# Kernel optimization log

Measured on AMD Instinct MI355X. Metric: run time of the kernel, lower is better.

The kernel has to match this reference:

```python
import jax, jax.numpy as jnp
import numpy as np

N, C, INTER = 8192, 256, 128


def setup_inputs() -> dict:
    key = jax.random.key(0)
    ks = jax.random.split(key, 9)
    s_in = 1.0 / np.sqrt(C)
    s_mid = 1.0 / np.sqrt(INTER)
    return {
        "x": jax.random.normal(ks[0], (N, C), dtype=jnp.float32),
        # weights stored [in, out] so projection is x @ w + b
        "g_w": jax.random.uniform(ks[1], (C, INTER), jnp.float32, -s_in, s_in),
        "g_b": jax.random.uniform(ks[2], (INTER,), jnp.float32, -s_in, s_in),
        "theta_w": jax.random.uniform(ks[3], (C, INTER), jnp.float32, -s_in, s_in),
        "theta_b": jax.random.uniform(ks[4], (INTER,), jnp.float32, -s_in, s_in),
        "phi_w": jax.random.uniform(ks[5], (C, INTER), jnp.float32, -s_in, s_in),
        "phi_b": jax.random.uniform(ks[6], (INTER,), jnp.float32, -s_in, s_in),
        "W_w": jax.random.uniform(ks[7], (INTER, C), jnp.float32, -s_mid, s_mid),
        "W_b": jax.random.uniform(ks[8], (C,), jnp.float32, -s_mid, s_mid),
    }


def reference(x, g_w, g_b, theta_w, theta_b, phi_w, phi_b, W_w, W_b):
    # embedded_gaussian variant; dropout treated as eval-mode identity
    g_x = x @ g_w + g_b            # [N, inter]
    theta_x = x @ theta_w + theta_b  # [N, inter]
    phi_x = x @ phi_w + phi_b        # [N, inter]
    f = theta_x @ phi_x.T            # [N, N] score matrix
    f_div_C = jax.nn.softmax(f, axis=-1)
    y = f_div_C @ g_x                # [N, inter]
    W_y = y @ W_w + W_b              # [N, C]
    return W_y + x
```

## Files before the change

kernel.cpp:

```cpp
#include <hip/hip_runtime.h>


typedef __bf16 bf16x8 __attribute__((ext_vector_type(8)));
typedef __bf16 bf16x4 __attribute__((ext_vector_type(4)));
typedef float f32x16 __attribute__((ext_vector_type(16)));

#define DEV __device__ __forceinline__

constexpr int NROW = 8192;
constexpr int CDIM = 256;
constexpr int DI   = 128;
constexpr int KVS  = 16;
constexpr int NIT  = NROW / KVS / 64;
constexpr float MFIX = 32.0f;
constexpr float LOG2E = 1.44269504f;

DEV int crow(int r, int h) { return (r & 3) + 8 * (r >> 2) + 4 * h; }

DEV f32x16 mfma(bf16x8 a, bf16x8 b, f32x16 c) {
    return __builtin_amdgcn_mfma_f32_32x32x16_bf16(a, b, c, 0, 0, 0);
}

DEV unsigned pack2(float a, float b) {
    union { __bf16 h[2]; unsigned u; } t;
    t.h[0] = (__bf16)a; t.h[1] = (__bf16)b;
    return t.u;
}

DEV void dma16(const void* g, void* l) {
    __builtin_amdgcn_global_load_lds(
        (const __attribute__((address_space(1))) unsigned*)g,
        (__attribute__((address_space(3))) unsigned*)l, 16, 0, 0);
}

__global__ void prep_wT(const float* __restrict__ thw, const float* __restrict__ phw,
                        const float* __restrict__ gw,  const float* __restrict__ Ww,
                        __bf16* __restrict__ thT, __bf16* __restrict__ phT,
                        __bf16* __restrict__ gT,  __bf16* __restrict__ WwT)
{
    const int m = blockIdx.y;
    const int o = blockIdx.x * 256 + threadIdx.x;
    if (m < 3) {
        const float* in = m == 0 ? thw : m == 1 ? phw : gw;
        __bf16* out = m == 0 ? thT : m == 1 ? phT : gT;
        int n = o >> 8, kk = o & 255;
        out[o] = (__bf16)in[kk * DI + n];
    } else {
        int c = o >> 7, kk = o & 127;
        WwT[o] = (__bf16)Ww[kk * CDIM + c];
    }
}

__global__ __launch_bounds__(256) void proj3(
    const float* __restrict__ x,
    const __bf16* __restrict__ thT, const float* __restrict__ thb,
    const __bf16* __restrict__ phT, const float* __restrict__ phb,
    const __bf16* __restrict__ gT,  const float* __restrict__ gb,
    __bf16* __restrict__ qo, __bf16* __restrict__ ko, __bf16* __restrict__ vT)
{
    const int which = blockIdx.y;
    const __bf16* wt  = which == 0 ? thT : which == 1 ? phT : gT;
    const float* bias = which == 0 ? thb : which == 1 ? phb : gb;
    const float osc   = which == 0 ? LOG2E : 1.0f;

    const int tid = threadIdx.x;
    const int wv = tid >> 6, lane = tid & 63, l31 = lane & 31, h = lane >> 5;
    const int rsel = wv & 1, csel = wv >> 1;

    if (which < 2) {
        __bf16* out = which == 0 ? qo : ko;
        const int row0 = blockIdx.x * 64 + rsel * 32;
        f32x16 acc[2] = {};
#pragma unroll
        for (int kk = 0; kk < 16; ++kk) {
            const float4* xp = (const float4*)(x + (size_t)(row0 + l31) * CDIM + kk * 16 + h * 8);
            float4 a0 = xp[0], a1 = xp[1];
            bf16x8 af;
            af[0] = (__bf16)a0.x; af[1] = (__bf16)a0.y; af[2] = (__bf16)a0.z; af[3] = (__bf16)a0.w;
            af[4] = (__bf16)a1.x; af[5] = (__bf16)a1.y; af[6] = (__bf16)a1.z; af[7] = (__bf16)a1.w;
#pragma unroll
            for (int jn = 0; jn < 2; ++jn) {
                int col0 = csel * 64 + jn * 32;
                bf16x8 bfr = *(const bf16x8*)(wt + (size_t)(col0 + l31) * CDIM + kk * 16 + h * 8);
                acc[jn] = mfma(af, bfr, acc[jn]);
            }
        }
#pragma unroll
        for (int jn = 0; jn < 2; ++jn) {
            int col = csel * 64 + jn * 32 + l31;
            float bv = bias[col];
#pragma unroll
            for (int r = 0; r < 16; ++r)
                out[(size_t)(row0 + crow(r, h)) * DI + col] = (__bf16)((acc[jn][r] + bv) * osc);
        }
    } else {
        const int xr0 = blockIdx.x * 64 + rsel * 32;
        f32x16 acc[2] = {};
#pragma unroll
        for (int kk = 0; kk < 16; ++kk) {
            const float4* xp = (const float4*)(x + (size_t)(xr0 + l31) * CDIM + kk * 16 + h * 8);
            float4 b0 = xp[0], b1 = xp[1];
            bf16x8 bf;
            bf[0] = (__bf16)b0.x; bf[1] = (__bf16)b0.y; bf[2] = (__bf16)b0.z; bf[3] = (__bf16)b0.w;
            bf[4] = (__bf16)b1.x; bf[5] = (__bf16)b1.y; bf[6] = (__bf16)b1.z; bf[7] = (__bf16)b1.w;
#pragma unroll
            for (int jn = 0; jn < 2; ++jn) {
                int i0 = csel * 64 + jn * 32;
                bf16x8 afr = *(const bf16x8*)(wt + (size_t)(i0 + l31) * CDIM + kk * 16 + h * 8);
                acc[jn] = mfma(afr, bf, acc[jn]);
            }
        }
#pragma unroll
        for (int jn = 0; jn < 2; ++jn) {
            int i0 = csel * 64 + jn * 32;
#pragma unroll
            for (int r = 0; r < 16; ++r) {
                int i = i0 + crow(r, h);
                vT[(size_t)i * NROW + xr0 + l31] = (__bf16)(acc[jn][r] + bias[i]);
            }
        }
    }
}

__global__ __launch_bounds__(256, 2) void flash(
    const __bf16* __restrict__ q, const __bf16* __restrict__ k,
    const __bf16* __restrict__ vT, __bf16* __restrict__ yac,
    float* __restrict__ mll)
{
    __shared__ __align__(16) __bf16 KtA[2][64 * 128];
    __shared__ __align__(16) __bf16 VtA[2][64 * 128];

    const int tid = threadIdx.x;
    const int wv = tid >> 6, lane = tid & 63, l31 = lane & 31, h = lane >> 5;
    const int bid = blockIdx.x;
    const int sp = bid & 15, qt = bid >> 4;
    const int q0 = qt * 128 + wv * 32;
    const int kvbase = sp * (NROW / KVS);

    bf16x8 qf[8];
#pragma unroll
    for (int kk = 0; kk < 8; ++kk)
        qf[kk] = *(const bf16x8*)(q + (size_t)(q0 + l31) * DI + kk * 16 + h * 8);

    f32x16 yacc[4] = {};
    float l = 0.f;

#define STAGE(Kt, Vt, kvb)                                                        \
    {                                                                             \
        _Pragma("unroll")                                                         \
        for (int rr = 0; rr < 4; ++rr) {                                          \
            int cix = rr * 256 + wv * 64 + lane;                                  \
            int r = cix >> 4, c = (cix & 15) ^ (r & 15);                          \
            dma16(k + (size_t)((kvb) + r) * DI + c * 8,                           \
                  (char*)(Kt) + rr * 4096 + wv * 1024);                           \
        }                                                                         \
        _Pragma("unroll")                                                         \
        for (int rr = 0; rr < 4; ++rr) {                                          \
            int cix = rr * 256 + wv * 64 + lane;                                  \
            int rw = cix >> 4, c = (cix & 15) ^ (rw & 15);                        \
            int d = rw * 2 + (c >> 3), kv8 = (c & 7) * 8;                         \
            dma16(vT + (size_t)d * NROW + (kvb) + kv8,                            \
                  (char*)(Vt) + rr * 4096 + wv * 1024);                           \
        }                                                                         \
    }

    STAGE(KtA[0], VtA[0], kvbase);
    __syncthreads();

    for (int it = 0; it < NIT; ++it) {
        const int cur = it & 1;
        if (it < NIT - 1) STAGE(KtA[cur ^ 1], VtA[cur ^ 1], kvbase + (it + 1) * 64);

        const __bf16* Kt = KtA[cur];
        const __bf16* Vt = VtA[cur];

        f32x16 sacc[2] = {};
        __builtin_amdgcn_s_setprio(1);
#pragma unroll
        for (int kk = 0; kk < 8; ++kk) {
#pragma unroll
            for (int jm = 0; jm < 2; ++jm) {
                int kv = jm * 32 + l31;
                bf16x8 kf = *(const bf16x8*)(&Kt[(kv * 128 + kk * 16 + h * 8) ^ ((kv & 15) << 3)]);
                sacc[jm] = mfma(kf, qf[kk], sacc[jm]);
            }
        }
        __builtin_amdgcn_s_setprio(0);

        float ts = 0.f;
#pragma unroll
        for (int jm = 0; jm < 2; ++jm)
#pragma unroll
            for (int r = 0; r < 16; ++r) {
                float p = exp2f(sacc[jm][r] - MFIX);
                sacc[jm][r] = p;
                ts += p;
            }
        ts += __shfl_xor(ts, 32);
        l += ts;

        bf16x8 pf[4];
#pragma unroll
        for (int ks = 0; ks < 4; ++ks) {
            const int jm = ks >> 1, r0 = 8 * (ks & 1);
            unsigned a0 = pack2(sacc[jm][r0],     sacc[jm][r0 + 1]);
            unsigned a1 = pack2(sacc[jm][r0 + 2], sacc[jm][r0 + 3]);
            unsigned b0 = pack2(sacc[jm][r0 + 4], sacc[jm][r0 + 5]);
            unsigned b1 = pack2(sacc[jm][r0 + 6], sacc[jm][r0 + 7]);
            unsigned snd0 = h ? a0 : b0, snd1 = h ? a1 : b1;
            unsigned loc0 = h ? b0 : a0, loc1 = h ? b1 : a1;
            unsigned rcv0 = (unsigned)__shfl_xor((int)snd0, 32);
            unsigned rcv1 = (unsigned)__shfl_xor((int)snd1, 32);
            union { unsigned w[4]; bf16x8 v; } pu;
            pu.w[0] = h ? rcv0 : loc0;
            pu.w[1] = h ? rcv1 : loc1;
            pu.w[2] = h ? loc0 : rcv0;
            pu.w[3] = h ? loc1 : rcv1;
            pf[ks] = pu.v;
        }

        __builtin_amdgcn_s_setprio(1);
#pragma unroll
        for (int jd = 0; jd < 4; ++jd) {
            int d = jd * 32 + l31, rw = d >> 1;
#pragma unroll
            for (int ks = 0; ks < 4; ++ks) {
                int co = (d & 1) * 64 + ks * 16 + h * 8;
                bf16x8 vf = *(const bf16x8*)(&Vt[(rw * 128 + co) ^ ((rw & 15) << 3)]);
                yacc[jd] = mfma(vf, pf[ks], yacc[jd]);
            }
        }
        __builtin_amdgcn_s_setprio(0);

        __syncthreads();
    }
#undef STAGE

    const size_t qrow = (size_t)sp * NROW + q0 + l31;
#pragma unroll
    for (int jd = 0; jd < 4; ++jd)
#pragma unroll
        for (int rq = 0; rq < 4; ++rq) {
            bf16x4 t;
#pragma unroll
            for (int i = 0; i < 4; ++i) t[i] = (__bf16)yacc[jd][rq * 4 + i];
            *(bf16x4*)(yac + qrow * DI + jd * 32 + rq * 8 + h * 4) = t;
        }
    if (h == 0) mll[sp * NROW + q0 + l31] = l;
}

__global__ __launch_bounds__(512) void merge_final(
    const __bf16* __restrict__ yac, const float* __restrict__ mll,
    const __bf16* __restrict__ WwT, const float* __restrict__ bias,
    const float* __restrict__ x, float* __restrict__ out)
{
    __shared__ __align__(16) __bf16 Yt[32 * 128];

    const int tid = threadIdx.x;
    const int row0 = blockIdx.x * 32;

    {
        const int qq = tid >> 4, ds = tid & 15;
        float L = 0.f;
#pragma unroll
        for (int s = 0; s < KVS; ++s) L += mll[s * NROW + row0 + qq];
        const float rL = 1.f / L;
        float fa[8] = {};
#pragma unroll
        for (int s = 0; s < KVS; ++s) {
            bf16x8 v = *(const bf16x8*)(yac + ((size_t)s * NROW + row0 + qq) * DI + ds * 8);
#pragma unroll
            for (int i = 0; i < 8; ++i) fa[i] += (float)v[i];
        }
        bf16x8 o;
#pragma unroll
        for (int i = 0; i < 8; ++i) o[i] = (__bf16)(fa[i] * rL);
        *(bf16x8*)(&Yt[(qq * 128 + ds * 8) ^ ((qq & 7) << 3)]) = o;
    }
    __syncthreads();

    const int wv = tid >> 6, lane = tid & 63, l31 = lane & 31, h = lane >> 5;
    bf16x8 af[8];
#pragma unroll
    for (int kk = 0; kk < 8; ++kk)
        af[kk] = *(const bf16x8*)(&Yt[(l31 * 128 + kk * 16 + h * 8) ^ ((l31 & 7) << 3)]);

    f32x16 acc = {};
#pragma unroll
    for (int kk = 0; kk < 8; ++kk) {
        bf16x8 bfr = *(const bf16x8*)(WwT + (size_t)(wv * 32 + l31) * DI + kk * 16 + h * 8);
        acc = mfma(af[kk], bfr, acc);
    }

    const int col = wv * 32 + l31;
    const float bv = bias[col];
#pragma unroll
    for (int r = 0; r < 16; ++r) {
        int row = row0 + crow(r, h);
        out[(size_t)row * CDIM + col] = acc[r] + bv + x[(size_t)row * CDIM + col];
    }
}

extern "C" void kernel_launch(void* const* d_in, const int* in_sizes, int n_in,
                              void* d_out, int out_size, void* d_ws, size_t ws_size,
                              hipStream_t stream)
{
    const float* x    = (const float*)d_in[0];
    const float* g_w  = (const float*)d_in[1];
    const float* g_b  = (const float*)d_in[2];
    const float* th_w = (const float*)d_in[3];
    const float* th_b = (const float*)d_in[4];
    const float* ph_w = (const float*)d_in[5];
    const float* ph_b = (const float*)d_in[6];
    const float* W_w  = (const float*)d_in[7];
    const float* W_b  = (const float*)d_in[8];
    float* out = (float*)d_out;

    char* ws = (char*)d_ws;
    __bf16* qws  = (__bf16*)(ws);
    __bf16* kws  = (__bf16*)(ws + (2ull << 20));
    __bf16* vTws = (__bf16*)(ws + (4ull << 20));
    __bf16* thT  = (__bf16*)(ws + (6ull << 20));
    __bf16* phT  = (__bf16*)(ws + (6ull << 20) + (64ull << 10));
    __bf16* gTw  = (__bf16*)(ws + (6ull << 20) + (128ull << 10));
    __bf16* WwT  = (__bf16*)(ws + (6ull << 20) + (192ull << 10));
    float*  mll  = (float*)(ws + (6ull << 20) + (256ull << 10));
    __bf16* yac  = (__bf16*)(ws + (7ull << 20));

    prep_wT<<<dim3(128, 4), 256, 0, stream>>>(th_w, ph_w, g_w, W_w, thT, phT, gTw, WwT);
    proj3<<<dim3(128, 3), 256, 0, stream>>>(x, thT, th_b, phT, ph_b, gTw, g_b,
                                            qws, kws, vTws);
    flash<<<1024, 256, 0, stream>>>(qws, kws, vTws, yac, mll);
    merge_final<<<256, 512, 0, stream>>>(yac, mll, WwT, W_b, x, out);
}
```

Measured before the change: 157.1 us.

## Fuse all four stages into one cooperative kernel with grid syncs

Replaces the four separate launches (weight transpose, projections, flash attention split, merge+output projection) with a single persistent cooperative kernel of 512 blocks that separates the phases with grid.sync(). It also precomputes LDS swizzle offsets and uses incrementing DMA source pointers instead of recomputing addresses each stage. This removes per-launch gaps and tail effects but forces 512 blocks to loop over 1024 flash tiles (two per block) and adds grid-wide barrier cost. The old multi-kernel path is kept as a fallback if the cooperative launch fails.

After: 370.2 us. 136% more time.

```diff
diff --git a/kernel.cpp b/kernel.cpp
--- a/kernel.cpp
+++ b/kernel.cpp
@@ -1,4 +1,5 @@
 #include <hip/hip_runtime.h>
+#include <hip/hip_cooperative_groups.h>
 
 
 typedef __bf16 bf16x8 __attribute__((ext_vector_type(8)));
@@ -31,6 +32,290 @@
     __builtin_amdgcn_global_load_lds(
         (const __attribute__((address_space(1))) unsigned*)g,
         (__attribute__((address_space(3))) unsigned*)l, 16, 0, 0);
+}
+
+__global__ __launch_bounds__(256, 2) void fused(
+    const float* __restrict__ x,
+    const float* __restrict__ g_w,  const float* __restrict__ g_b,
+    const float* __restrict__ th_w, const float* __restrict__ th_b,
+    const float* __restrict__ ph_w, const float* __restrict__ ph_b,
+    const float* __restrict__ W_w,  const float* __restrict__ W_b,
+    float* __restrict__ out,
+    __bf16* __restrict__ qws, __bf16* __restrict__ kws, __bf16* __restrict__ vTws,
+    __bf16* __restrict__ thT, __bf16* __restrict__ phT, __bf16* __restrict__ gTw,
+    __bf16* __restrict__ WwT, float* __restrict__ mll, __bf16* __restrict__ yac)
+{
+    __shared__ __align__(16) __bf16 KtA[2][64 * 128];
+    __shared__ __align__(16) __bf16 VtA[2][64 * 128];
+
+    auto grid = cooperative_groups::this_grid();
+    const int bid = blockIdx.x, tid = threadIdx.x;
+    const int wv = tid >> 6, lane = tid & 63, l31 = lane & 31, h = lane >> 5;
+
+    {
+        int o = bid * 256 + tid;
+        int m = o >> 15, o15 = o & 32767;
+        if (m < 3) {
+            const float* in = m == 0 ? th_w : m == 1 ? ph_w : g_w;
+            __bf16* ow      = m == 0 ? thT  : m == 1 ? phT  : gTw;
+            int n = o15 >> 8, kk = o15 & 255;
+            ow[o15] = (__bf16)in[kk * DI + n];
+        } else {
+            int c = o15 >> 7, kk = o15 & 127;
+            WwT[o15] = (__bf16)W_w[kk * CDIM + c];
+        }
+    }
+    grid.sync();
+
+    if (bid < 384) {
+        const int which = bid >> 7, bx = bid & 127;
+        const __bf16* wt  = which == 0 ? thT : which == 1 ? phT : gTw;
+        const float* bias = which == 0 ? th_b : which == 1 ? ph_b : g_b;
+        const int rsel = wv & 1, csel = wv >> 1;
+
+        if (which < 2) {
+            __bf16* o = which == 0 ? qws : kws;
+            const float osc = which == 0 ? LOG2E : 1.0f;
+            const int row0 = bx * 64 + rsel * 32;
+            f32x16 acc[2] = {};
+#pragma unroll
+            for (int kk = 0; kk < 16; ++kk) {
+                const float4* xp = (const float4*)(x + (size_t)(row0 + l31) * CDIM + kk * 16 + h * 8);
+                float4 a0 = xp[0], a1 = xp[1];
+                bf16x8 af;
+                af[0] = (__bf16)a0.x; af[1] = (__bf16)a0.y; af[2] = (__bf16)a0.z; af[3] = (__bf16)a0.w;
+                af[4] = (__bf16)a1.x; af[5] = (__bf16)a1.y; af[6] = (__bf16)a1.z; af[7] = (__bf16)a1.w;
+#pragma unroll
+                for (int jn = 0; jn < 2; ++jn) {
+                    int col0 = csel * 64 + jn * 32;
+                    bf16x8 bfr = *(const bf16x8*)(wt + (size_t)(col0 + l31) * CDIM + kk * 16 + h * 8);
+                    acc[jn] = mfma(af, bfr, acc[jn]);
+                }
+            }
+#pragma unroll
+            for (int jn = 0; jn < 2; ++jn) {
+                int col = csel * 64 + jn * 32 + l31;
+                float bv = bias[col];
+#pragma unroll
+                for (int r = 0; r < 16; ++r)
+                    o[(size_t)(row0 + crow(r, h)) * DI + col] = (__bf16)((acc[jn][r] + bv) * osc);
+            }
+        } else {
+            const int xr0 = bx * 64 + rsel * 32;
+            f32x16 acc[2] = {};
+#pragma unroll
+            for (int kk = 0; kk < 16; ++kk) {
+                const float4* xp = (const float4*)(x + (size_t)(xr0 + l31) * CDIM + kk * 16 + h * 8);
+                float4 b0 = xp[0], b1 = xp[1];
+                bf16x8 bf;
+                bf[0] = (__bf16)b0.x; bf[1] = (__bf16)b0.y; bf[2] = (__bf16)b0.z; bf[3] = (__bf16)b0.w;
+                bf[4] = (__bf16)b1.x; bf[5] = (__bf16)b1.y; bf[6] = (__bf16)b1.z; bf[7] = (__bf16)b1.w;
+#pragma unroll
+                for (int jn = 0; jn < 2; ++jn) {
+                    int i0 = csel * 64 + jn * 32;
+                    bf16x8 afr = *(const bf16x8*)(wt + (size_t)(i0 + l31) * CDIM + kk * 16 + h * 8);
+                    acc[jn] = mfma(afr, bf, acc[jn]);
+                }
+            }
+#pragma unroll
+            for (int jn = 0; jn < 2; ++jn) {
+                int i0 = csel * 64 + jn * 32;
+#pragma unroll
+                for (int r = 0; r < 16; ++r) {
+                    int i = i0 + crow(r, h);
+                    vTws[(size_t)i * NROW + xr0 + l31] = (__bf16)(acc[jn][r] + bias[i]);
+                }
+            }
+        }
+    }
+    grid.sync();
+
+    int koff[16], voff[16];
+#pragma unroll
+    for (int kk = 0; kk < 8; ++kk)
+#pragma unroll
+        for (int jm = 0; jm < 2; ++jm) {
+            int kv = jm * 32 + l31;
+            koff[kk * 2 + jm] = (kv * 128 + kk * 16 + h * 8) ^ ((kv & 15) << 3);
+        }
+#pragma unroll
+    for (int jd = 0; jd < 4; ++jd)
+#pragma unroll
+        for (int ks = 0; ks < 4; ++ks) {
+            int d = jd * 32 + l31, rw = d >> 1;
+            voff[jd * 4 + ks] = (rw * 128 + (d & 1) * 64 + ks * 16 + h * 8) ^ ((rw & 15) << 3);
+        }
+
+    for (int t = bid; t < 1024; t += 512) {
+        const int sp = t & 15, qt = t >> 4;
+        const int q0 = qt * 128 + wv * 32;
+        const int kvbase = sp * (NROW / KVS);
+
+        bf16x8 qf[8];
+#pragma unroll
+        for (int kk = 0; kk < 8; ++kk)
+            qf[kk] = *(const bf16x8*)(qws + (size_t)(q0 + l31) * DI + kk * 16 + h * 8);
+
+        const __bf16* kSrc[4];
+        const __bf16* vSrc[4];
+#pragma unroll
+        for (int rr = 0; rr < 4; ++rr) {
+            int cix = rr * 256 + wv * 64 + lane;
+            int r = cix >> 4, c = (cix & 15) ^ (r & 15);
+            kSrc[rr] = kws + (size_t)(kvbase + r) * DI + c * 8;
+            int d = r * 2 + (c >> 3), kv8 = (c & 7) * 8;
+            vSrc[rr] = vTws + (size_t)d * NROW + kvbase + kv8;
+        }
+
+#define STAGE(KT, VT)                                                         \
+    {                                                                         \
+        _Pragma("unroll")                                                     \
+        for (int rr = 0; rr < 4; ++rr) {                                      \
+            dma16(kSrc[rr], (char*)(KT) + rr * 4096 + wv * 1024);             \
+            kSrc[rr] += 64 * DI;                                              \
+        }                                                                     \
+        _Pragma("unroll")                                                     \
+        for (int rr = 0; rr < 4; ++rr) {                                      \
+            dma16(vSrc[rr], (char*)(VT) + rr * 4096 + wv * 1024);             \
+            vSrc[rr] += 64;                                                   \
+        }                                                                     \
+    }
+
+        f32x16 yacc[4] = {};
+        float l = 0.f;
+
+        STAGE(KtA[0], VtA[0]);
+        __syncthreads();
+
+        for (int it = 0; it < NIT; ++it) {
+            const int cur = it & 1;
+            if (it < NIT - 1) STAGE(KtA[cur ^ 1], VtA[cur ^ 1]);
+
+            const __bf16* Kt = KtA[cur];
+            const __bf16* Vt = VtA[cur];
+
+            f32x16 sacc[2] = {};
+            __builtin_amdgcn_s_setprio(1);
+#pragma unroll
+            for (int kk = 0; kk < 8; ++kk)
+#pragma unroll
+                for (int jm = 0; jm < 2; ++jm) {
+                    bf16x8 kf = *(const bf16x8*)(&Kt[koff[kk * 2 + jm]]);
+                    sacc[jm] = mfma(kf, qf[kk], sacc[jm]);
+                }
+            __builtin_amdgcn_s_setprio(0);
+
+            float ts = 0.f;
+#pragma unroll
+            for (int jm = 0; jm < 2; ++jm)
+#pragma unroll
+                for (int r = 0; r < 16; ++r) {
+                    float p = exp2f(sacc[jm][r] - MFIX);
+                    sacc[jm][r] = p;
+                    ts += p;
+                }
+            ts += __shfl_xor(ts, 32);
+            l += ts;
+
+            bf16x8 pf[4];
+#pragma unroll
+            for (int ks = 0; ks < 4; ++ks) {
+                const int jm = ks >> 1, r0 = 8 * (ks & 1);
+                unsigned a0 = pack2(sacc[jm][r0],     sacc[jm][r0 + 1]);
+                unsigned a1 = pack2(sacc[jm][r0 + 2], sacc[jm][r0 + 3]);
+                unsigned b0 = pack2(sacc[jm][r0 + 4], sacc[jm][r0 + 5]);
+                unsigned b1 = pack2(sacc[jm][r0 + 6], sacc[jm][r0 + 7]);
+                unsigned snd0 = h ? a0 : b0, snd1 = h ? a1 : b1;
+                unsigned loc0 = h ? b0 : a0, loc1 = h ? b1 : a1;
+                unsigned rcv0 = (unsigned)__shfl_xor((int)snd0, 32);
+                unsigned rcv1 = (unsigned)__shfl_xor((int)snd1, 32);
+                union { unsigned w[4]; bf16x8 v; } pu;
+                pu.w[0] = h ? rcv0 : loc0;
+                pu.w[1] = h ? rcv1 : loc1;
+                pu.w[2] = h ? loc0 : rcv0;
+                pu.w[3] = h ? loc1 : rcv1;
+                pf[ks] = pu.v;
+            }
+
+            __builtin_amdgcn_s_setprio(1);
+#pragma unroll
+            for (int jd = 0; jd < 4; ++jd)
+#pragma unroll
+                for (int ks = 0; ks < 4; ++ks) {
+                    bf16x8 vf = *(const bf16x8*)(&Vt[voff[jd * 4 + ks]]);
+                    yacc[jd] = mfma(vf, pf[ks], yacc[jd]);
+                }
+            __builtin_amdgcn_s_setprio(0);
+
+            __syncthreads();
+        }
+#undef STAGE
+
+        const size_t qrow = (size_t)sp * NROW + q0 + l31;
+#pragma unroll
+        for (int jd = 0; jd < 4; ++jd)
+#pragma unroll
+            for (int rq = 0; rq < 4; ++rq) {
+                bf16x4 tb;
+#pragma unroll
+                for (int i = 0; i < 4; ++i) tb[i] = (__bf16)yacc[jd][rq * 4 + i];
+                *(bf16x4*)(yac + qrow * DI + jd * 32 + rq * 8 + h * 4) = tb;
+            }
+        if (h == 0) mll[sp * NROW + q0 + l31] = l;
+    }
+    grid.sync();
+    __syncthreads();
+
+    {
+        __bf16* Yt = (__bf16*)KtA;
+        const int rt = bid >> 1, ch = bid & 1;
+        const int row0 = rt * 32;
+
+        {
+            const int qq = tid >> 3, ds = tid & 7;
+            float L = 0.f;
+#pragma unroll
+            for (int s = 0; s < KVS; ++s) L += mll[s * NROW + row0 + qq];
+            const float rL = 1.f / L;
+            float fa[16] = {};
+#pragma unroll
+            for (int s = 0; s < KVS; ++s) {
+                const __bf16* p = yac + ((size_t)s * NROW + row0 + qq) * DI + ds * 16;
+                bf16x8 v0 = *(const bf16x8*)p;
+                bf16x8 v1 = *(const bf16x8*)(p + 8);
+#pragma unroll
+                for (int i = 0; i < 8; ++i) { fa[i] += (float)v0[i]; fa[8 + i] += (float)v1[i]; }
+            }
+            bf16x8 o0, o1;
+#pragma unroll
+            for (int i = 0; i < 8; ++i) { o0[i] = (__bf16)(fa[i] * rL); o1[i] = (__bf16)(fa[8 + i] * rL); }
+            int base = qq * 128 + ds * 16;
+            *(bf16x8*)(&Yt[base ^ ((qq & 7) << 3)])       = o0;
+            *(bf16x8*)(&Yt[(base + 8) ^ ((qq & 7) << 3)]) = o1;
+        }
+        __syncthreads();
+
+        bf16x8 af[8];
+#pragma unroll
+        for (int kk = 0; kk < 8; ++kk)
+            af[kk] = *(const bf16x8*)(&Yt[(l31 * 128 + kk * 16 + h * 8) ^ ((l31 & 7) << 3)]);
+
+        const int col0 = ch * 128 + wv * 32;
+        f32x16 acc = {};
+#pragma unroll
+        for (int kk = 0; kk < 8; ++kk) {
+            bf16x8 bfr = *(const bf16x8*)(WwT + (size_t)(col0 + l31) * DI + kk * 16 + h * 8);
+            acc = mfma(af[kk], bfr, acc);
+        }
+
+        const int col = col0 + l31;
+        const float bv = W_b[col];
+#pragma unroll
+        for (int r = 0; r < 16; ++r) {
+            int row = row0 + crow(r, h);
+            out[(size_t)row * CDIM + col] = acc[r] + bv + x[(size_t)row * CDIM + col];
+        }
+    }
 }
 
 __global__ void prep_wT(const float* __restrict__ thw, const float* __restrict__ phw,
@@ -61,14 +346,13 @@
     const int which = blockIdx.y;
     const __bf16* wt  = which == 0 ? thT : which == 1 ? phT : gT;
     const float* bias = which == 0 ? thb : which == 1 ? phb : gb;
-    const float osc   = which == 0 ? LOG2E : 1.0f;
-
     const int tid = threadIdx.x;
     const int wv = tid >> 6, lane = tid & 63, l31 = lane & 31, h = lane >> 5;
     const int rsel = wv & 1, csel = wv >> 1;
 
     if (which < 2) {
-        __bf16* out = which == 0 ? qo : ko;
+        __bf16* o = which == 0 ? qo : ko;
+        const float osc = which == 0 ? LOG2E : 1.0f;
         const int row0 = blockIdx.x * 64 + rsel * 32;
         f32x16 acc[2] = {};
 #pragma unroll
@@ -91,7 +375,7 @@
             float bv = bias[col];
 #pragma unroll
             for (int r = 0; r < 16; ++r)
-                out[(size_t)(row0 + crow(r, h)) * DI + col] = (__bf16)((acc[jn][r] + bv) * osc);
+                o[(size_t)(row0 + crow(r, h)) * DI + col] = (__bf16)((acc[jn][r] + bv) * osc);
         }
     } else {
         const int xr0 = blockIdx.x * 64 + rsel * 32;
@@ -145,31 +429,37 @@
     f32x16 yacc[4] = {};
     float l = 0.f;
 
-#define STAGE(Kt, Vt, kvb)                                                        \
-    {                                                                             \
-        _Pragma("unroll")                                                         \
-        for (int rr = 0; rr < 4; ++rr) {                                          \
-            int cix = rr * 256 + wv * 64 + lane;                                  \
-            int r = cix >> 4, c = (cix & 15) ^ (r & 15);                          \
-            dma16(k + (size_t)((kvb) + r) * DI + c * 8,                           \
-                  (char*)(Kt) + rr * 4096 + wv * 1024);                           \
-        }                                                                         \
-        _Pragma("unroll")                                                         \
-        for (int rr = 0; rr < 4; ++rr) {                                          \
-            int cix = rr * 256 + wv * 64 + lane;                                  \
-            int rw = cix >> 4, c = (cix & 15) ^ (rw & 15);                        \
-            int d = rw * 2 + (c >> 3), kv8 = (c & 7) * 8;                         \
-            dma16(vT + (size_t)d * NROW + (kvb) + kv8,                            \
-                  (char*)(Vt) + rr * 4096 + wv * 1024);                           \
-        }                                                                         \
-    }
-
-    STAGE(KtA[0], VtA[0], kvbase);
+    const __bf16* kSrc[4];
+    const __bf16* vSrc[4];
+#pragma unroll
+    for (int rr = 0; rr < 4; ++rr) {
+        int cix = rr * 256 + wv * 64 + lane;
+        int r = cix >> 4, c = (cix & 15) ^ (r & 15);
+        kSrc[rr] = k + (size_t)(kvbase + r) * DI + c * 8;
+        int d = r * 2 + (c >> 3), kv8 = (c & 7) * 8;
+        vSrc[rr] = vT + (size_t)d * NROW + kvbase + kv8;
+    }
+
+#define STAGE(KT, VT)                                                         \
+    {                                                                         \
+        _Pragma("unroll")                                                     \
+        for (int rr = 0; rr < 4; ++rr) {                                      \
+            dma16(kSrc[rr], (char*)(KT) + rr * 4096 + wv * 1024);             \
+            kSrc[rr] += 64 * DI;                                              \
+        }                                                                     \
+        _Pragma("unroll")                                                     \
+        for (int rr = 0; rr < 4; ++rr) {                                      \
+            dma16(vSrc[rr], (char*)(VT) + rr * 4096 + wv * 1024);             \
+            vSrc[rr] += 64;                                                   \
+        }                                                                     \
+    }
+
+    STAGE(KtA[0], VtA[0]);
     __syncthreads();
 
     for (int it = 0; it < NIT; ++it) {
         const int cur = it & 1;
-        if (it < NIT - 1) STAGE(KtA[cur ^ 1], VtA[cur ^ 1], kvbase + (it + 1) * 64);
+        if (it < NIT - 1) STAGE(KtA[cur ^ 1], VtA[cur ^ 1]);
 
         const __bf16* Kt = KtA[cur];
         const __bf16* Vt = VtA[cur];
@@ -177,14 +467,13 @@
         f32x16 sacc[2] = {};
         __builtin_amdgcn_s_setprio(1);
 #pragma unroll
-        for (int kk = 0; kk < 8; ++kk) {
+        for (int kk = 0; kk < 8; ++kk)
 #pragma unroll
             for (int jm = 0; jm < 2; ++jm) {
                 int kv = jm * 32 + l31;
                 bf16x8 kf = *(const bf16x8*)(&Kt[(kv * 128 + kk * 16 + h * 8) ^ ((kv & 15) << 3)]);
                 sacc[jm] = mfma(kf, qf[kk], sacc[jm]);
             }
-        }
         __builtin_amdgcn_s_setprio(0);
 
         float ts = 0.f;
@@ -241,10 +530,10 @@
     for (int jd = 0; jd < 4; ++jd)
 #pragma unroll
         for (int rq = 0; rq < 4; ++rq) {
-            bf16x4 t;
-#pragma unroll
-            for (int i = 0; i < 4; ++i) t[i] = (__bf16)yacc[jd][rq * 4 + i];
-            *(bf16x4*)(yac + qrow * DI + jd * 32 + rq * 8 + h * 4) = t;
+            bf16x4 tb;
+#pragma unroll
+            for (int i = 0; i < 4; ++i) tb[i] = (__bf16)yacc[jd][rq * 4 + i];
+            *(bf16x4*)(yac + qrow * DI + jd * 32 + rq * 8 + h * 4) = tb;
         }
     if (h == 0) mll[sp * NROW + q0 + l31] = l;
 }
@@ -327,9 +616,20 @@
     float*  mll  = (float*)(ws + (6ull << 20) + (256ull << 10));
     __bf16* yac  = (__bf16*)(ws + (7ull << 20));
 
-    prep_wT<<<dim3(128, 4), 256, 0, stream>>>(th_w, ph_w, g_w, W_w, thT, phT, gTw, WwT);
-    proj3<<<dim3(128, 3), 256, 0, stream>>>(x, thT, th_b, phT, ph_b, gTw, g_b,
-                                            qws, kws, vTws);
-    flash<<<1024, 256, 0, stream>>>(qws, kws, vTws, yac, mll);
-    merge_final<<<256, 512, 0, stream>>>(yac, mll, WwT, W_b, x, out);
-}
+    void* args[] = {
+        (void*)&x, (void*)&g_w, (void*)&g_b, (void*)&th_w, (void*)&th_b,
+        (void*)&ph_w, (void*)&ph_b, (void*)&W_w, (void*)&W_b, (void*)&out,
+        (void*)&qws, (void*)&kws, (void*)&vTws, (void*)&thT, (void*)&phT,
+        (void*)&gTw, (void*)&WwT, (void*)&mll, (void*)&yac
+    };
+    hipError_t e = hipLaunchCooperativeKernel((const void*)fused, dim3(512),
+                                              dim3(256), args, 0, stream);
+    if (e != hipSuccess) {
+        prep_wT<<<dim3(128, 4), 256, 0, stream>>>(th_w, ph_w, g_w, W_w,
+                                                  thT, phT, gTw, WwT);
+        proj3<<<dim3(128, 3), 256, 0, stream>>>(x, thT, th_b, phT, ph_b,
+                                                gTw, g_b, qws, kws, vTws);
+        flash<<<1024, 256, 0, stream>>>(qws, kws, vTws, yac, mll);
+        merge_final<<<256, 512, 0, stream>>>(yac, mll, WwT, W_b, x, out);
+    }
+}
```
